# Optimization experiments

Measured on AMD Instinct MI355X. Metric: run time of the kernel, lower is better.

Reference implementation:

```python
import jax, jax.numpy as jnp
import numpy as np

N, INT_DIM = 4096, 512
X_DIMS = [128, 128, 128, 128]
DIM_LIST = list(zip(X_DIMS[:-1], X_DIMS[1:]))
TOT_DIM = sum(d0 * d1 + d1 for d0, d1 in DIM_LIST)  # 49536
FUNS = [jax.nn.relu, jax.nn.relu, None]


def setup_inputs() -> dict:
    key = jax.random.key(0)
    k1, k2, k3, k4 = jax.random.split(key, 4)
    int_x = jax.random.normal(k1, (N, INT_DIM), dtype=jnp.float32)
    x = jax.random.normal(k2, (N, X_DIMS[0]), dtype=jnp.float32)
    # torch Linear(IntDim, tot_dim): W [out, in], b [out]; scale like kaiming-uniform-ish
    W = jax.random.normal(k3, (TOT_DIM, INT_DIM), dtype=jnp.float32) * (1.0 / np.sqrt(INT_DIM))
    b = jax.random.normal(k4, (TOT_DIM,), dtype=jnp.float32) * 0.02
    return {"int_x": int_x, "x": x, "W": W, "b": b}


def reference(int_x, x, W, b):
    # hypernetwork: per-sample generated weights/biases, [N, tot_dim]
    temp = jnp.einsum('ni,oi->no', int_x, W) + b
    cum = 0
    h = x
    for (d0, d1), fun in zip(DIM_LIST, FUNS):
        bias = temp[:, cum:cum + d1]                                   # [N, d1]
        weight = temp[:, cum + d1:cum + d1 + d0 * d1].reshape(-1, d0, d1)  # [N, d0, d1]
        cum += d1 + d0 * d1
        h = jnp.einsum('npq,np->nq', weight, h) + bias
        if fun is not None:
            h = fun(h)
    return h
```

## Files before the change

kernel.cpp:

```cpp
#include <hip/hip_runtime.h>
#include <cstdint>
#include <cstddef>

#define NSAMP 4096
#define KDIM  512
#define TOT   49536

typedef __attribute__((ext_vector_type(8))) __bf16 bf16x8;
typedef __attribute__((ext_vector_type(4))) __bf16 bf16x4;
typedef __attribute__((ext_vector_type(4))) float  f32x4;

__global__ void cast_bf16(const float* __restrict__ in, __bf16* __restrict__ out, int n4) {
    int i = blockIdx.x * blockDim.x + threadIdx.x;
    int stride = gridDim.x * blockDim.x;
    for (; i < n4; i += stride) {
        float4 v = ((const float4*)in)[i];
        bf16x4 o = { (__bf16)v.x, (__bf16)v.y, (__bf16)v.z, (__bf16)v.w };
        ((bf16x4*)out)[i] = o;
    }
}

__global__ __launch_bounds__(256) void hyper_gemm(
    const __bf16* __restrict__ A, const __bf16* __restrict__ B,
    const float* __restrict__ bias, __bf16* __restrict__ C)
{
    __shared__ __bf16 As[128 * 32];
    __shared__ __bf16 Bs[128 * 32];

    const int tid   = threadIdx.x;
    const int lane  = tid & 63;
    const int wv    = tid >> 6;
    const int quad  = lane >> 4;
    const int r16   = lane & 15;
    const int waveM = wv >> 1;
    const int waveN = wv & 1;

    const int m0 = blockIdx.y * 128;
    const int n0 = blockIdx.x * 128;

    f32x4 acc[4][4] = {};

    for (int kt = 0; kt < KDIM / 32; ++kt) {
        const int k0 = kt * 32;
#pragma unroll
        for (int c = 0; c < 2; ++c) {
            int idx = (wv * 2 + c) * 64 + lane;
            int row = idx >> 2;
            int col = (idx & 3) << 3;
            const __bf16* ga = A + (size_t)(m0 + row) * KDIM + (k0 + col);
            __builtin_amdgcn_global_load_lds(
                (__attribute__((address_space(1))) void*)ga,
                (__attribute__((address_space(3))) void*)(As + (wv * 2 + c) * 512),
                16, 0, 0);
            const __bf16* gb = B + (size_t)(n0 + row) * KDIM + (k0 + col);
            __builtin_amdgcn_global_load_lds(
                (__attribute__((address_space(1))) void*)gb,
                (__attribute__((address_space(3))) void*)(Bs + (wv * 2 + c) * 512),
                16, 0, 0);
        }
        __syncthreads();

        bf16x8 af[4], bf[4];
#pragma unroll
        for (int i = 0; i < 4; ++i)
            af[i] = *(const bf16x8*)(As + (waveM * 64 + i * 16 + r16) * 32 + quad * 8);
#pragma unroll
        for (int j = 0; j < 4; ++j)
            bf[j] = *(const bf16x8*)(Bs + (waveN * 64 + j * 16 + r16) * 32 + quad * 8);

#pragma unroll
        for (int i = 0; i < 4; ++i)
#pragma unroll
            for (int j = 0; j < 4; ++j)
                acc[i][j] = __builtin_amdgcn_mfma_f32_16x16x32_bf16(af[i], bf[j], acc[i][j], 0, 0, 0);
        __syncthreads();
    }

#pragma unroll
    for (int j = 0; j < 4; ++j) {
        int n = n0 + waveN * 64 + j * 16 + r16;
        float bb = bias[n];
#pragma unroll
        for (int i = 0; i < 4; ++i) {
            int mbase = m0 + waveM * 64 + i * 16 + quad * 4;
#pragma unroll
            for (int rr = 0; rr < 4; ++rr) {
                C[(size_t)(mbase + rr) * TOT + n] = (__bf16)(acc[i][j][rr] + bb);
            }
        }
    }
}

__global__ __launch_bounds__(256) void mlp_kernel(
    const float* __restrict__ x, const __bf16* __restrict__ temp,
    float* __restrict__ out, int samp0)
{
    const int n   = samp0 + blockIdx.x;
    const int tid = threadIdx.x;
    const int wv  = tid >> 6;
    const int l   = tid & 63;
    const int pg  = l >> 4;
    const int qg  = l & 15;

    __shared__ float h[128];
    __shared__ float partial[4][128];

    if (tid < 64) ((float2*)h)[tid] = ((const float2*)(x + (size_t)n * 128))[tid];

    const __bf16* row = temp + (size_t)blockIdx.x * TOT;
    int cum = 0;
#pragma unroll
    for (int layer = 0; layer < 3; ++layer) {
        const __bf16* bias = row + cum;
        const __bf16* wgt  = row + cum + 128;
        float acc[8] = {0, 0, 0, 0, 0, 0, 0, 0};
        __syncthreads();
#pragma unroll
        for (int i = 0; i < 8; ++i) {
            int p = wv * 32 + i * 4 + pg;
            bf16x8 w = *(const bf16x8*)(wgt + (size_t)p * 128 + qg * 8);
            float hp = h[p];
#pragma unroll
            for (int j = 0; j < 8; ++j) acc[j] += (float)w[j] * hp;
        }
#pragma unroll
        for (int j = 0; j < 8; ++j) {
            acc[j] += __shfl_xor(acc[j], 16);
            acc[j] += __shfl_xor(acc[j], 32);
        }
        if (pg == 0) {
#pragma unroll
            for (int j = 0; j < 8; ++j) partial[wv][qg * 8 + j] = acc[j];
        }
        __syncthreads();
        if (tid < 128) {
            float v = partial[0][tid] + partial[1][tid] + partial[2][tid] + partial[3][tid]
                    + (float)bias[tid];
            if (layer < 2) v = fmaxf(v, 0.f);
            h[tid] = v;
        }
        cum += 128 + 128 * 128;
    }
    __syncthreads();
    if (tid < 64) ((float2*)(out + (size_t)n * 128))[tid] = ((const float2*)h)[tid];
}

extern "C" void kernel_launch(void* const* d_in, const int* in_sizes, int n_in,
                              void* d_out, int out_size, void* d_ws, size_t ws_size,
                              hipStream_t stream) {
    const float* int_x = (const float*)d_in[0];
    const float* x     = (const float*)d_in[1];
    const float* W     = (const float*)d_in[2];
    const float* b     = (const float*)d_in[3];
    float* out = (float*)d_out;

    char* ws = (char*)d_ws;
    __bf16* A_bf = (__bf16*)ws;
    size_t offA = (size_t)NSAMP * KDIM * 2;
    __bf16* W_bf = (__bf16*)(ws + offA);
    size_t offW = offA + (size_t)TOT * KDIM * 2;
    __bf16* temp = (__bf16*)(ws + offW);

    size_t remain = (ws_size > offW) ? (ws_size - offW) : 0;
    int chunk = 128;
    for (int c = 1024; c >= 128; c >>= 1) {
        if ((size_t)c * TOT * 2 <= remain) { chunk = c; break; }
    }

    int nA4 = NSAMP * KDIM / 4;
    cast_bf16<<<(nA4 + 255) / 256, 256, 0, stream>>>(int_x, A_bf, nA4);
    int nW4 = TOT * KDIM / 4;
    cast_bf16<<<(nW4 + 255) / 256, 256, 0, stream>>>(W, W_bf, nW4);

    for (int samp0 = 0; samp0 < NSAMP; samp0 += chunk) {
        dim3 grid(TOT / 128, chunk / 128);
        hyper_gemm<<<grid, 256, 0, stream>>>(A_bf + (size_t)samp0 * KDIM, W_bf, b, temp);
        mlp_kernel<<<chunk, 256, 0, stream>>>(x, temp, out, samp0);
    }
}
```

Measured before the change: 581.8 us.

## Swizzle LDS layout, group tile raster order, and raise hyper_gemm occupancy hint

Applies an XOR swizzle to the 16-byte chunks of each row in the A/B shared-memory tiles, so fragment reads from LDS avoid bank conflicts. Remaps block indices into column groups 48 tiles wide so concurrently running blocks share W tiles in L2. It also sets the launch_bounds minimum blocks per SM to 4, which may constrain register allocation. The raster remap adds some integer index arithmetic per block.

```diff
diff --git a/kernel.cpp b/kernel.cpp
--- a/kernel.cpp
+++ b/kernel.cpp
@@ -5,6 +5,7 @@
 #define NSAMP 4096
 #define KDIM  512
 #define TOT   49536
+#define NUMN  387
 
 typedef __attribute__((ext_vector_type(8))) __bf16 bf16x8;
 typedef __attribute__((ext_vector_type(4))) __bf16 bf16x4;
@@ -20,7 +21,7 @@
     }
 }
 
-__global__ __launch_bounds__(256) void hyper_gemm(
+__global__ __launch_bounds__(256, 4) void hyper_gemm(
     const __bf16* __restrict__ A, const __bf16* __restrict__ B,
     const float* __restrict__ bias, __bf16* __restrict__ C)
 {
@@ -35,24 +36,37 @@
     const int waveM = wv >> 1;
     const int waveN = wv & 1;
 
-    const int m0 = blockIdx.y * 128;
-    const int n0 = blockIdx.x * 128;
+    const int num_m = gridDim.y;
+    const int hw    = blockIdx.y * NUMN + blockIdx.x;
+    const int STW   = 48;
+    const int gsize = STW * num_m;
+    const int group = hw / gsize;
+    const int local = hw % gsize;
+    const int n_base = group * STW;
+    int width = NUMN - n_base; if (width > STW) width = STW;
+    const int m_t = local / width;
+    const int n_t = n_base + local % width;
+
+    const int m0 = m_t * 128;
+    const int n0 = n_t * 128;
 
     f32x4 acc[4][4] = {};
+
+    const int rsw = (r16 >> 1) & 3;
 
     for (int kt = 0; kt < KDIM / 32; ++kt) {
         const int k0 = kt * 32;
 #pragma unroll
         for (int c = 0; c < 2; ++c) {
-            int idx = (wv * 2 + c) * 64 + lane;
-            int row = idx >> 2;
-            int col = (idx & 3) << 3;
-            const __bf16* ga = A + (size_t)(m0 + row) * KDIM + (k0 + col);
+            int idx  = (wv * 2 + c) * 64 + lane;
+            int row  = idx >> 2;
+            int gsrc = (idx & 3) ^ ((row >> 1) & 3);
+            const __bf16* ga = A + (size_t)(m0 + row) * KDIM + (k0 + gsrc * 8);
             __builtin_amdgcn_global_load_lds(
                 (__attribute__((address_space(1))) void*)ga,
                 (__attribute__((address_space(3))) void*)(As + (wv * 2 + c) * 512),
                 16, 0, 0);
-            const __bf16* gb = B + (size_t)(n0 + row) * KDIM + (k0 + col);
+            const __bf16* gb = B + (size_t)(n0 + row) * KDIM + (k0 + gsrc * 8);
             __builtin_amdgcn_global_load_lds(
                 (__attribute__((address_space(1))) void*)gb,
                 (__attribute__((address_space(3))) void*)(Bs + (wv * 2 + c) * 512),
@@ -62,11 +76,15 @@
 
         bf16x8 af[4], bf[4];
 #pragma unroll
-        for (int i = 0; i < 4; ++i)
-            af[i] = *(const bf16x8*)(As + (waveM * 64 + i * 16 + r16) * 32 + quad * 8);
+        for (int i = 0; i < 4; ++i) {
+            int r = waveM * 64 + i * 16 + r16;
+            af[i] = *(const bf16x8*)(As + r * 32 + (quad ^ rsw) * 8);
+        }
 #pragma unroll
-        for (int j = 0; j < 4; ++j)
-            bf[j] = *(const bf16x8*)(Bs + (waveN * 64 + j * 16 + r16) * 32 + quad * 8);
+        for (int j = 0; j < 4; ++j) {
+            int r = waveN * 64 + j * 16 + r16;
+            bf[j] = *(const bf16x8*)(Bs + r * 32 + (quad ^ rsw) * 8);
+        }
 
 #pragma unroll
         for (int i = 0; i < 4; ++i)
@@ -173,7 +191,7 @@
     cast_bf16<<<(nW4 + 255) / 256, 256, 0, stream>>>(W, W_bf, nW4);
 
     for (int samp0 = 0; samp0 < NSAMP; samp0 += chunk) {
-        dim3 grid(TOT / 128, chunk / 128);
+        dim3 grid(NUMN, chunk / 128);
         hyper_gemm<<<grid, 256, 0, stream>>>(A_bf + (size_t)samp0 * KDIM, W_bf, b, temp);
         mlp_kernel<<<chunk, 256, 0, stream>>>(x, temp, out, samp0);
     }
```

Measured after the change: 597.1 us. 2.6% more time.
